# Kernel tuning notes

Measured on AMD Instinct MI355X. Metric: run time of the kernel, lower is better.

The kernel has to match this reference:

```python
import jax, jax.numpy as jnp
import numpy as np
from jax import lax

B, H, W = 16, 512, 512
K, C, D = 64, 512, 256  # num_clusters, feature channels, descriptor_dim


def conv2d(x, w, b, stride, pad):
    y = lax.conv_general_dilated(x, w, (stride, stride), ((pad, pad), (pad, pad)),
                                 dimension_numbers=("NCHW", "OIHW", "NCHW"))
    return y + b[None, :, None, None]


def maxpool2(x):
    return lax.reduce_window(x, -jnp.inf, lax.max, (1, 1, 2, 2), (1, 1, 2, 2), "VALID")


def setup_inputs() -> dict:
    key = jax.random.key(0)
    ks = jax.random.split(key, 16)
    def rn(k, shape, fan_in):
        return jax.random.normal(k, shape, jnp.float32) * (1.0 / np.sqrt(fan_in))
    return {
        "x": jax.random.normal(ks[0], (B, 3, H, W), jnp.float32),
        "w1": rn(ks[1], (64, 3, 3, 3), 27), "b1": jnp.zeros((64,), jnp.float32),
        "w2": rn(ks[2], (128, 64, 3, 3), 576), "b2": jnp.zeros((128,), jnp.float32),
        "w3": rn(ks[3], (256, 128, 3, 3), 1152), "b3": jnp.zeros((256,), jnp.float32),
        "w4": rn(ks[4], (512, 256, 3, 3), 2304), "b4": jnp.zeros((512,), jnp.float32),
        "wv": rn(ks[5], (K, C), C), "bv": jnp.zeros((K,), jnp.float32),
        "centroids": jax.random.normal(ks[6], (K, C), jnp.float32),
        "fw1": rn(ks[7], (D, K * C), K * C), "fb1": jnp.zeros((D,), jnp.float32),
        "fw2": rn(ks[8], (D, D), D), "fb2": jnp.zeros((D,), jnp.float32),
    }


def reference(x, w1, b1, w2, b2, w3, b3, w4, b4, wv, bv, centroids, fw1, fb1, fw2, fb2):
    # conv backbone (SimpleGlobalDescriptor.backbone)
    h = jax.nn.relu(conv2d(x, w1, b1, 2, 1)); h = maxpool2(h)
    h = jax.nn.relu(conv2d(h, w2, b2, 2, 1)); h = maxpool2(h)
    h = jax.nn.relu(conv2d(h, w3, b3, 2, 1)); h = maxpool2(h)
    h = jax.nn.relu(conv2d(h, w4, b4, 2, 1))
    feats = jnp.mean(h, axis=(2, 3))  # AdaptiveAvgPool2d((1,1)) -> (B, C)
    # NetVLAD soft assignment: 1x1 conv + softmax over cluster dim
    logits = jnp.einsum("bc,kc->bk", feats, wv) + bv  # (B, K)
    a = jax.nn.softmax(logits, axis=1)  # spatial N == 1 after avgpool
    # fused VLAD: a[:,k] * (feats - centroids[k]) summed over N(=1)
    # == a (outer) feats - a[:,:,None] * centroids
    vlad = a[:, :, None] * (feats[:, None, :] - centroids[None, :, :])  # (B, K, C)
    v = vlad.reshape(B, K * C)
    # final descriptor MLP + L2 norm
    d = jax.nn.relu(v @ fw1.T + fb1) @ fw2.T + fb2
    d = d / jnp.linalg.norm(d, axis=1, keepdims=True)
    return d
```

## Files before the change

kernel.cpp:

```cpp
#include <hip/hip_runtime.h>
#include <hip/hip_bf16.h>

typedef unsigned short ushort_t;
typedef short bf16x8 __attribute__((ext_vector_type(8)));
typedef float f32x4 __attribute__((ext_vector_type(4)));

__device__ __forceinline__ ushort_t f2b(float f) {
    __hip_bfloat16 h = __float2bfloat16(f);
    return *reinterpret_cast<ushort_t*>(&h);
}
__device__ __forceinline__ float b2f(short v) {
    union { unsigned int u; float f; } cv;
    cv.u = ((unsigned int)(ushort_t)v) << 16;
    return cv.f;
}

__global__ __launch_bounds__(256) void k_packall(const float* __restrict__ w1,
                                                 const float* __restrict__ w2,
                                                 const float* __restrict__ w3,
                                                 const float* __restrict__ w4,
                                                 ushort_t* __restrict__ o1,
                                                 ushort_t* __restrict__ o2,
                                                 ushort_t* __restrict__ o3,
                                                 ushort_t* __restrict__ o4m) {
    const int bx = blockIdx.x;
    if (bx < 512) {
        const int co = bx;
        __shared__ float sw[2304];
        for (int i = threadIdx.x; i < 2304; i += 256) sw[i] = w4[(size_t)co * 2304 + i];
        __syncthreads();
        const int g = co >> 4, l15 = co & 15;
        for (int it = threadIdx.x; it < 288; it += 256) {
            const int kc = it >> 2, kg = it & 3;
            const int k0 = kc * 32 + kg * 8;
            const int tap = k0 >> 8, ci0 = k0 & 255;
            const int lane = kg * 16 + l15;
            ushort_t tmp[8];
#pragma unroll
            for (int j = 0; j < 8; ++j)
                tmp[j] = f2b(sw[(ci0 + j) * 9 + tap]);
            *(float4*)(o4m + ((size_t)(kc * 32 + g) * 64 + lane) * 8) = *(const float4*)tmp;
        }
    } else if (bx < 656) {
        const int slot = (bx - 512) * 256 + threadIdx.x;
        const int lane = slot & 63, g = (slot >> 6) & 15, kc = slot >> 10;
        const int k0 = kc * 32 + ((lane >> 4) << 3);
        const int tap = k0 >> 7, cib = k0 & 127;
        const int ky = tap >= 6 ? 2 : (tap >= 3 ? 1 : 0), kx = tap - ky * 3;
        const int co = g * 16 + (lane & 15);
#pragma unroll
        for (int j = 0; j < 8; ++j)
            o3[slot * 8 + j] = f2b(w3[((co * 128 + cib + j) * 3 + ky) * 3 + kx]);
    } else if (bx < 692) {
        const int slot = (bx - 656) * 256 + threadIdx.x;
        const int lane = slot & 63, g = (slot >> 6) & 7, kc = slot >> 9;
        const int k0 = kc * 32 + ((lane >> 4) << 3);
        const int tap = k0 >> 6, sb = k0 & 63;
        const int ky = tap >= 6 ? 2 : (tap >= 3 ? 1 : 0), kx = tap - ky * 3;
        const int co = g * 16 + (lane & 15);
#pragma unroll
        for (int j = 0; j < 8; ++j) {
            const int s = sb + j;
            const int ci = 16 * (s & 3) + (s >> 2);
            o2[slot * 8 + j] = f2b(w2[((co * 64 + ci) * 3 + ky) * 3 + kx]);
        }
    } else {
        const int slot = threadIdx.x;
        const int lane = slot & 63, nf = slot >> 6;
        const int co = nf * 16 + (lane & 15);
        const int kg = lane >> 4;
#pragma unroll
        for (int j = 0; j < 8; ++j) {
            const int k = kg * 8 + j;
            float v = 0.f;
            if (k < 27) {
                const int t = k / 3, c = k - 3 * t;
                v = w1[(co * 3 + c) * 9 + t];
            }
            o1[slot * 8 + j] = f2b(v);
        }
    }
}

__global__ __launch_bounds__(256) void k_conv1f(const float* __restrict__ x,
                                                const ushort_t* __restrict__ wpk1,
                                                const float* __restrict__ b1,
                                                ushort_t* __restrict__ y1) {
    const int rp = blockIdx.x, xh = blockIdx.y, b = blockIdx.z;
    const int tid = threadIdx.x;
    const int wid = tid >> 6, lane = tid & 63;
    const int l15 = lane & 15, kg = lane >> 4;

    __shared__ __align__(16) ushort_t sX[3 * 9 * 260];
    const float* xb = x + (size_t)b * 3 * 512 * 512;
    const int iy0 = 8 * rp - 1;
    const int ix0 = 256 * xh - 1;
#pragma unroll
    for (int c = 0; c < 3; ++c)
#pragma unroll
    for (int r = 0; r < 9; ++r) {
        const int iy = iy0 + r;
        const int ix = ix0 + tid;
        float v = 0.f;
        if (iy >= 0 && ix >= 0) v = xb[((size_t)c * 512 + iy) * 512 + ix];
        sX[(c * 9 + r) * 260 + tid] = f2b(v);
    }
    if (tid < 27) {
        const int c = tid / 9, r = tid - 9 * c;
        const int iy = iy0 + r, ix = ix0 + 256;
        float v = (iy >= 0) ? xb[((size_t)c * 512 + iy) * 512 + ix] : 0.f;
        sX[(c * 9 + r) * 260 + 256] = f2b(v);
    }
    __syncthreads();

    const int kbase = kg * 8;
#define OFFJ(J) __extension__ ({ int k_ = kbase + (J); if (k_ > 26) k_ = 26; \
        const int tap_ = k_ / 3; const int c_ = k_ - 3 * tap_; \
        const int ky_ = tap_ / 3; const int kx_ = tap_ - 3 * ky_; \
        c_ * 2340 + ky_ * 260 + kx_; })
    const int o0 = OFFJ(0), o1 = OFFJ(1), o2 = OFFJ(2), o3 = OFFJ(3);
    const int o4 = OFFJ(4), o5 = OFFJ(5), o6 = OFFJ(6), o7 = OFFJ(7);
#undef OFFJ
    const int gq = l15 >> 2;
    const int dy = (l15 >> 1) & 1, dx = l15 & 1;

    bf16x8 bF[4];
    float bias[4];
#pragma unroll
    for (int nf = 0; nf < 4; ++nf) {
        bF[nf] = *reinterpret_cast<const bf16x8*>(wpk1 + (size_t)(nf * 64 + lane) * 8);
        bias[nf] = b1[nf * 16 + l15];
    }
    const f32x4 z4 = {0.f, 0.f, 0.f, 0.f};

#pragma unroll 4
    for (int it = 0; it < 8; ++it) {
        const int fl = wid * 8 + it;
        const int g2 = fl * 4 + gq;
        const int pyl = g2 >> 6, pxl = g2 & 63;
        const int cr = 2 * pyl + dy;
        const int oxl = 2 * pxl + dx;
        const int base = cr * 520 + 2 * oxl;
        bf16x8 aF;
        aF[0] = (short)sX[base + o0];
        aF[1] = (short)sX[base + o1];
        aF[2] = (short)sX[base + o2];
        aF[3] = (short)sX[base + o3];
        aF[4] = (short)sX[base + o4];
        aF[5] = (short)sX[base + o5];
        aF[6] = (short)sX[base + o6];
        aF[7] = (short)sX[base + o7];
        f32x4 acc[4];
#pragma unroll
        for (int nf = 0; nf < 4; ++nf)
            acc[nf] = __builtin_amdgcn_mfma_f32_16x16x32_bf16(aF, bF[nf], z4, 0, 0, 0);
        const int g_out = fl * 4 + kg;
        const int pyo = g_out >> 6, pxo = xh * 64 + (g_out & 63);
        union { ushort_t u[4]; uint2 v; } pk;
#pragma unroll
        for (int nf = 0; nf < 4; ++nf) {
            float v = fmaxf(fmaxf(acc[nf][0], acc[nf][1]), fmaxf(acc[nf][2], acc[nf][3]));
            pk.u[nf] = f2b(fmaxf(v + bias[nf], 0.f));
        }
        *(uint2*)(y1 + ((size_t)(b * 128 + 2 * rp + pyo) * 128 + pxo) * 64 + 4 * l15) = pk.v;
    }
}

__global__ __launch_bounds__(256) void k_conv2s(const ushort_t* __restrict__ y1,
                                                const ushort_t* __restrict__ wpk2,
                                                const float* __restrict__ b2,
                                                ushort_t* __restrict__ y2) {
    const int b = blockIdx.z;
    const int xh = blockIdx.y;
    const int rp = blockIdx.x;
    const int tid = threadIdx.x;
    const int wid = tid >> 6, lane = tid & 63;
    const int l15 = lane & 15, kg = lane >> 4;

    __shared__ __align__(16) ushort_t sY[330 * 72];
    bf16x8* sYv = (bf16x8*)sY;

    const ushort_t* xb = y1 + (size_t)b * 128 * 128 * 64;
    const int iyb = 4 * rp - 1, ixb = 64 * xh - 1;
    for (int j = tid; j < 2640; j += 256) {
        const int q = j & 7;
        const int pc = j >> 3;
        const int cc = pc % 66, r = pc / 66;
        const int iy = iyb + r, ix = ixb + cc;
        bf16x8 v = {0, 0, 0, 0, 0, 0, 0, 0};
        if (iy >= 0 && ix >= 0 && ix < 128)
            v = *reinterpret_cast<const bf16x8*>(xb + ((size_t)iy * 128 + ix) * 64 + q * 8);
        sYv[pc * 9 + (q ^ ((pc >> 1) & 7))] = v;
    }
    __syncthreads();

    const f32x4 z4 = {0.f, 0.f, 0.f, 0.f};
    f32x4 acc[2][2][2];
#pragma unroll
    for (int i = 0; i < 2; ++i)
#pragma unroll
        for (int j = 0; j < 2; ++j) { acc[i][j][0] = z4; acc[i][j][1] = z4; }

#pragma unroll 1
    for (int tap = 0; tap < 9; ++tap) {
        const int ky = tap >= 6 ? 2 : (tap >= 3 ? 1 : 0), kx = tap - ky * 3;
#pragma unroll
        for (int h = 0; h < 2; ++h) {
            const int kc = tap * 2 + h;
            const int c8 = h * 4 + kg;
            bf16x8 aF[2][2];
#pragma unroll
            for (int oyi = 0; oyi < 2; ++oyi)
#pragma unroll
            for (int m2 = 0; m2 < 2; ++m2) {
                const int r = 2 * oyi + ky;
                const int cc = 2 * l15 + m2 * 32 + kx;
                const int pc = r * 66 + cc;
                aF[oyi][m2] = sYv[pc * 9 + (c8 ^ ((pc >> 1) & 7))];
            }
            bf16x8 bF[2];
#pragma unroll
            for (int nf = 0; nf < 2; ++nf)
                bF[nf] = *reinterpret_cast<const bf16x8*>(wpk2 + ((size_t)(kc * 8 + wid * 2 + nf) * 64 + lane) * 8);
#pragma unroll
            for (int oyi = 0; oyi < 2; ++oyi)
#pragma unroll
            for (int m2 = 0; m2 < 2; ++m2)
#pragma unroll
            for (int nf = 0; nf < 2; ++nf)
                acc[oyi][m2][nf] = __builtin_amdgcn_mfma_f32_16x16x32_bf16(aF[oyi][m2], bF[nf], acc[oyi][m2][nf], 0, 0, 0);
        }
    }
    const int kgx = lane >> 4;
#pragma unroll
    for (int nf = 0; nf < 2; ++nf) {
        const int co = wid * 32 + nf * 16 + l15;
        const float bias = b2[co];
#pragma unroll
        for (int m2 = 0; m2 < 2; ++m2)
#pragma unroll
            for (int p = 0; p < 2; ++p) {
                float v = fmaxf(fmaxf(acc[0][m2][nf][2 * p], acc[0][m2][nf][2 * p + 1]),
                                fmaxf(acc[1][m2][nf][2 * p], acc[1][m2][nf][2 * p + 1]));
                const int px = (xh * 2 + m2) * 8 + kgx * 2 + p;
                y2[((size_t)(b * 32 + rp) * 32 + px) * 128 + co] = f2b(fmaxf(v + bias, 0.f));
            }
    }
}

__global__ __launch_bounds__(256) void k_conv3m(const ushort_t* __restrict__ y2,
                                                const ushort_t* __restrict__ wpk3,
                                                const float* __restrict__ b3,
                                                ushort_t* __restrict__ y3) {
    const int gy = blockIdx.x, gn = blockIdx.y, b = blockIdx.z;
    const int oy0 = gy * 4;
    const int tid = threadIdx.x;
    const int wid = tid >> 6, lane = tid & 63;
    const int l15 = lane & 15, kl8 = (lane >> 4) << 3;
    const int g16 = gn * 4 + wid;
    const int co = g16 * 16 + l15;

    const ushort_t* xb = y2 + (size_t)b * 32 * 32 * 128;
    const f32x4 z4 = {0.f, 0.f, 0.f, 0.f};
    f32x4 acc[4] = {z4, z4, z4, z4};

#pragma unroll 1
    for (int tap = 0; tap < 9; ++tap) {
        const int ky = tap >= 6 ? 2 : (tap >= 3 ? 1 : 0), kx = tap - ky * 3;
        const int iyA = 2 * oy0 - 1 + ky;
        const int c = 2 * l15 - 1 + kx;
        const bool cok = (c >= 0);
#pragma unroll
        for (int h = 0; h < 4; ++h) {
            const int ci0 = h * 32;
            const int kc = tap * 4 + h;
            bf16x8 aF[4];
#pragma unroll
            for (int mf = 0; mf < 4; ++mf) {
                const int iy = iyA + 2 * mf;
                bf16x8 r = {0, 0, 0, 0, 0, 0, 0, 0};
                if (cok && iy >= 0) r = *reinterpret_cast<const bf16x8*>(xb + ((size_t)iy * 32 + c) * 128 + ci0 + kl8);
                aF[mf] = r;
            }
            const bf16x8 bF = *reinterpret_cast<const bf16x8*>(wpk3 + ((size_t)(kc * 16 + g16) * 64 + lane) * 8);
#pragma unroll
            for (int mf = 0; mf < 4; ++mf)
                acc[mf] = __builtin_amdgcn_mfma_f32_16x16x32_bf16(aF[mf], bF, acc[mf], 0, 0, 0);
        }
    }
    const int kg = lane >> 4;
    const float bias = b3[co];
#pragma unroll
    for (int mp = 0; mp < 2; ++mp) {
        const int py = gy * 2 + mp;
#pragma unroll
        for (int p = 0; p < 2; ++p) {
            float v = fmaxf(fmaxf(acc[2 * mp][2 * p], acc[2 * mp][2 * p + 1]),
                            fmaxf(acc[2 * mp + 1][2 * p], acc[2 * mp + 1][2 * p + 1]));
            const int px = kg * 2 + p;
            y3[((size_t)(b * 8 + py) * 8 + px) * 256 + co] = f2b(fmaxf(v + bias, 0.f));
        }
    }
}

__global__ __launch_bounds__(256) void k_conv4g(const ushort_t* __restrict__ y3,
                                                const ushort_t* __restrict__ wpk4m,
                                                const float* __restrict__ b4,
                                                float* __restrict__ feats) {
    const int g16 = blockIdx.x, b = blockIdx.y;
    const int tid = threadIdx.x, wid = tid >> 6, lane = tid & 63;
    const int l15 = lane & 15, kg = lane >> 4, kl8 = kg << 3;
    const int oy = l15 >> 2, ox = l15 & 3;
    const f32x4 z4 = {0.f, 0.f, 0.f, 0.f};
    f32x4 acc = z4;
    const ushort_t* yb = y3 + (size_t)b * 16384;
    const int kc0 = wid * 18;

#pragma unroll 3
    for (int i = 0; i < 18; ++i) {
        const int kc = kc0 + i;
        const int k0 = kc * 32 + kl8;
        const int tap = k0 >> 8, ci0 = k0 & 255;
        const int ky = tap / 3, kx = tap - 3 * (tap / 3);
        const int iy = 2 * oy - 1 + ky, ix = 2 * ox - 1 + kx;
        bf16x8 aF = {0, 0, 0, 0, 0, 0, 0, 0};
        if (iy >= 0 && ix >= 0)
            aF = *reinterpret_cast<const bf16x8*>(yb + ((iy * 8 + ix) << 8) + ci0);
        const bf16x8 bF = *reinterpret_cast<const bf16x8*>(wpk4m + ((size_t)(kc * 32 + g16) * 64 + lane) * 8);
        acc = __builtin_amdgcn_mfma_f32_16x16x32_bf16(aF, bF, acc, 0, 0, 0);
    }

    __shared__ f32x4 red[4][64];
    red[wid][lane] = acc;
    __syncthreads();
    if (wid == 0) {
        f32x4 t = red[0][lane];
        t = t + red[1][lane];
        t = t + red[2][lane];
        t = t + red[3][lane];
        const int co = g16 * 16 + l15;
        const float bias = b4[co];
        float s = fmaxf(t[0] + bias, 0.f) + fmaxf(t[1] + bias, 0.f)
                + fmaxf(t[2] + bias, 0.f) + fmaxf(t[3] + bias, 0.f);
        s += __shfl_xor(s, 16, 64);
        s += __shfl_xor(s, 32, 64);
        if (kg == 0) feats[b * 512 + co] = s * 0.0625f;
    }
}

__global__ __launch_bounds__(256) void k_head(const float* __restrict__ feats,
                                              const float* __restrict__ wv,
                                              const float* __restrict__ bv,
                                              const float* __restrict__ centroids,
                                              float* __restrict__ v) {
    const int b = blockIdx.x, sl8 = blockIdx.y;
    __shared__ float sf[512];
    __shared__ float sl[64];
    __shared__ float sa[64];
    for (int i = threadIdx.x; i < 512; i += 256) sf[i] = feats[b * 512 + i];
    __syncthreads();
    if (threadIdx.x < 64) {
        const int k = threadIdx.x;
        float s = bv[k];
        for (int c = 0; c < 512; ++c) s += sf[c] * wv[(size_t)k * 512 + c];
        sl[k] = s;
    }
    __syncthreads();
    if (threadIdx.x < 64) {
        const int k = threadIdx.x;
        float m = -1e30f;
        for (int i = 0; i < 64; ++i) m = fmaxf(m, sl[i]);
        float sum = 0.f;
        for (int i = 0; i < 64; ++i) sum += __expf(sl[i] - m);
        sa[k] = __expf(sl[k] - m) / sum;
    }
    __syncthreads();
    const int i4end = (sl8 + 1) * 4096;
    for (int i4 = sl8 * 4096 + threadIdx.x * 4; i4 < i4end; i4 += 1024) {
        const int k = i4 >> 9;
        const float a_ = sa[k];
        const float4 c4 = *(const float4*)(centroids + i4);
        const float4 f4 = *(const float4*)(&sf[i4 & 511]);
        float4 o;
        o.x = a_ * (f4.x - c4.x);
        o.y = a_ * (f4.y - c4.y);
        o.z = a_ * (f4.z - c4.z);
        o.w = a_ * (f4.w - c4.w);
        *(float4*)(v + (size_t)b * 32768 + i4) = o;
    }
}

__global__ __launch_bounds__(256) void k_fc1m(const float* __restrict__ v,
                                              const float* __restrict__ fw1,
                                              float* __restrict__ part) {
    const int g16 = blockIdx.x, by = blockIdx.y;
    const int tid = threadIdx.x, wid = tid >> 6, lane = tid & 63;
    const int l15 = lane & 15, kg = lane >> 4;
    const f32x4 z4 = {0.f, 0.f, 0.f, 0.f};
    f32x4 acc = z4;
    const float* vrow = v + (size_t)l15 * 32768;
    const float* wrow = fw1 + (size_t)(g16 * 16 + l15) * 32768;
    const int kc0 = by * 16 + wid * 4;

#pragma unroll
    for (int i = 0; i < 4; ++i) {
        const int j0 = (kc0 + i) * 32 + kg * 8;
        const float4 va = *(const float4*)(vrow + j0);
        const float4 vb = *(const float4*)(vrow + j0 + 4);
        const float4 wa = *(const float4*)(wrow + j0);
        const float4 wb = *(const float4*)(wrow + j0 + 4);
        bf16x8 aF, bF;
        aF[0] = (short)f2b(va.x); aF[1] = (short)f2b(va.y);
        aF[2] = (short)f2b(va.z); aF[3] = (short)f2b(va.w);
        aF[4] = (short)f2b(vb.x); aF[5] = (short)f2b(vb.y);
        aF[6] = (short)f2b(vb.z); aF[7] = (short)f2b(vb.w);
        bF[0] = (short)f2b(wa.x); bF[1] = (short)f2b(wa.y);
        bF[2] = (short)f2b(wa.z); bF[3] = (short)f2b(wa.w);
        bF[4] = (short)f2b(wb.x); bF[5] = (short)f2b(wb.y);
        bF[6] = (short)f2b(wb.z); bF[7] = (short)f2b(wb.w);
        acc = __builtin_amdgcn_mfma_f32_16x16x32_bf16(aF, bF, acc, 0, 0, 0);
    }

    __shared__ f32x4 red[4][64];
    red[wid][lane] = acc;
    __syncthreads();
    if (wid == 0) {
        f32x4 t = red[0][lane];
        t = t + red[1][lane];
        t = t + red[2][lane];
        t = t + red[3][lane];
#pragma unroll
        for (int r = 0; r < 4; ++r)
            part[((size_t)by * 16 + (kg * 4 + r)) * 256 + g16 * 16 + l15] = t[r];
    }
}

__global__ __launch_bounds__(256) void k_fc2(const float* __restrict__ part,
                                             const float* __restrict__ fb1,
                                             const float* __restrict__ fw2,
                                             const float* __restrict__ fb2,
                                             float* __restrict__ out) {
    const int b = blockIdx.x;
    const int dd = threadIdx.x;
    __shared__ float sd[256];
    __shared__ float sq[256];
    float t = fb1[dd];
#pragma unroll 8
    for (int ks = 0; ks < 64; ++ks) t += part[((size_t)ks * 16 + b) * 256 + dd];
    sd[dd] = fmaxf(t, 0.f);
    __syncthreads();
    float s = fb2[dd];
    for (int j = 0; j < 256; ++j) s += sd[j] * fw2[(size_t)dd * 256 + j];
    sq[dd] = s * s;
    __syncthreads();
    for (int off = 128; off >= 1; off >>= 1) {
        if (dd < off) sq[dd] += sq[dd + off];
        __syncthreads();
    }
    const float inv = rsqrtf(sq[0]);
    out[b * 256 + dd] = s * inv;
}

extern "C" void kernel_launch(void* const* d_in, const int* in_sizes, int n_in,
                              void* d_out, int out_size, void* d_ws, size_t ws_size,
                              hipStream_t stream) {
    const float* x    = (const float*)d_in[0];
    const float* w1   = (const float*)d_in[1];
    const float* b1   = (const float*)d_in[2];
    const float* w2   = (const float*)d_in[3];
    const float* b2   = (const float*)d_in[4];
    const float* w3   = (const float*)d_in[5];
    const float* b3   = (const float*)d_in[6];
    const float* w4   = (const float*)d_in[7];
    const float* b4   = (const float*)d_in[8];
    const float* wv   = (const float*)d_in[9];
    const float* bv   = (const float*)d_in[10];
    const float* cen  = (const float*)d_in[11];
    const float* fw1  = (const float*)d_in[12];
    const float* fb1  = (const float*)d_in[13];
    const float* fw2  = (const float*)d_in[14];
    const float* fb2  = (const float*)d_in[15];
    float* out = (float*)d_out;

    char* p = (char*)d_ws;
    ushort_t* y1    = (ushort_t*)p; p += 33554432;
    ushort_t* wpk2  = (ushort_t*)p; p += 147456;
    ushort_t* wpk3  = (ushort_t*)p; p += 589824;
    ushort_t* wpk4m = (ushort_t*)p; p += 2359296;
    ushort_t* wpk1  = (ushort_t*)p; p += 4096;
    ushort_t* y2    = (ushort_t*)p; p += 4194304;
    ushort_t* y3    = (ushort_t*)p; p += 524288;
    float*    feats = (float*)p;    p += 32768;
    float*    vbuf  = (float*)p;    p += 2097152;
    float*    part  = (float*)p;    p += 1048576;

    k_packall<<<693, 256, 0, stream>>>(w1, w2, w3, w4, wpk1, wpk2, wpk3, wpk4m);
    k_conv1f<<<dim3(64, 2, 16), 256, 0, stream>>>(x, wpk1, b1, y1);
    k_conv2s<<<dim3(32, 2, 16), 256, 0, stream>>>(y1, wpk2, b2, y2);
    k_conv3m<<<dim3(4, 4, 16), 256, 0, stream>>>(y2, wpk3, b3, y3);
    k_conv4g<<<dim3(32, 16), 256, 0, stream>>>(y3, wpk4m, b4, feats);
    k_head<<<dim3(16, 8), 256, 0, stream>>>(feats, wv, bv, cen, vbuf);
    k_fc1m<<<dim3(16, 64), 256, 0, stream>>>(vbuf, fw1, part);
    k_fc2<<<16, 256, 0, stream>>>(part, fb1, fw2, fb2, out);
}
```

Baseline: 115.4 us.

## Interleave conv1 input channels in LDS and store VLAD vector as bf16

Conv1's shared-memory tile now interleaves the three input channels per pixel, and the packed weight K ordering is reordered to (ky, kx, c). Each MFMA A fragment is then read with four 32-bit loads from contiguous LDS instead of eight scattered 16-bit gathers, with a special path for the three leftover taps. Separately, the VLAD head writes bf16 instead of fp32, which halves that buffer's traffic and drops the conversion in fc1. The risk is extra divergence in the kg==3 branch and possible unaligned 32-bit LDS reads at odd offsets.

```diff
diff --git a/kernel.cpp b/kernel.cpp
--- a/kernel.cpp
+++ b/kernel.cpp
@@ -73,9 +73,13 @@
         for (int j = 0; j < 8; ++j) {
             const int k = kg * 8 + j;
             float v = 0.f;
-            if (k < 27) {
-                const int t = k / 3, c = k - 3 * t;
-                v = w1[(co * 3 + c) * 9 + t];
+            if (k < 24) {
+                const int ky = k >> 3, q = k & 7;
+                const int kx = q / 3, c = q - 3 * kx;
+                v = w1[(co * 3 + c) * 9 + ky * 3 + kx];
+            } else if (k < 27) {
+                const int ky = k - 24;
+                v = w1[(co * 3 + 2) * 9 + ky * 3 + 2];
             }
             o1[slot * 8 + j] = f2b(v);
         }
@@ -91,7 +95,7 @@
     const int wid = tid >> 6, lane = tid & 63;
     const int l15 = lane & 15, kg = lane >> 4;
 
-    __shared__ __align__(16) ushort_t sX[3 * 9 * 260];
+    __shared__ __align__(16) ushort_t sX[9 * 776];
     const float* xb = x + (size_t)b * 3 * 512 * 512;
     const int iy0 = 8 * rp - 1;
     const int ix0 = 256 * xh - 1;
@@ -103,24 +107,16 @@
         const int ix = ix0 + tid;
         float v = 0.f;
         if (iy >= 0 && ix >= 0) v = xb[((size_t)c * 512 + iy) * 512 + ix];
-        sX[(c * 9 + r) * 260 + tid] = f2b(v);
+        sX[r * 776 + tid * 3 + c] = f2b(v);
     }
     if (tid < 27) {
         const int c = tid / 9, r = tid - 9 * c;
         const int iy = iy0 + r, ix = ix0 + 256;
         float v = (iy >= 0) ? xb[((size_t)c * 512 + iy) * 512 + ix] : 0.f;
-        sX[(c * 9 + r) * 260 + 256] = f2b(v);
-    }
-    __syncthreads();
-
-    const int kbase = kg * 8;
-#define OFFJ(J) __extension__ ({ int k_ = kbase + (J); if (k_ > 26) k_ = 26; \
-        const int tap_ = k_ / 3; const int c_ = k_ - 3 * tap_; \
-        const int ky_ = tap_ / 3; const int kx_ = tap_ - 3 * ky_; \
-        c_ * 2340 + ky_ * 260 + kx_; })
-    const int o0 = OFFJ(0), o1 = OFFJ(1), o2 = OFFJ(2), o3 = OFFJ(3);
-    const int o4 = OFFJ(4), o5 = OFFJ(5), o6 = OFFJ(6), o7 = OFFJ(7);
-#undef OFFJ
+        sX[r * 776 + 256 * 3 + c] = f2b(v);
+    }
+    __syncthreads();
+
     const int gq = l15 >> 2;
     const int dy = (l15 >> 1) & 1, dx = l15 & 1;
 
@@ -140,16 +136,20 @@
         const int pyl = g2 >> 6, pxl = g2 & 63;
         const int cr = 2 * pyl + dy;
         const int oxl = 2 * pxl + dx;
-        const int base = cr * 520 + 2 * oxl;
         bf16x8 aF;
-        aF[0] = (short)sX[base + o0];
-        aF[1] = (short)sX[base + o1];
-        aF[2] = (short)sX[base + o2];
-        aF[3] = (short)sX[base + o3];
-        aF[4] = (short)sX[base + o4];
-        aF[5] = (short)sX[base + o5];
-        aF[6] = (short)sX[base + o6];
-        aF[7] = (short)sX[base + o7];
+        if (kg < 3) {
+            const int ba = (2 * cr + kg) * 776 + 6 * oxl;
+            const unsigned int* pu = (const unsigned int*)(sX + ba);
+            union { unsigned int u[4]; bf16x8 v; } cvt;
+            cvt.u[0] = pu[0]; cvt.u[1] = pu[1]; cvt.u[2] = pu[2]; cvt.u[3] = pu[3];
+            aF = cvt.v;
+        } else {
+            const int b0 = 2 * cr * 776 + 6 * oxl + 8;
+            aF = (bf16x8){0, 0, 0, 0, 0, 0, 0, 0};
+            aF[0] = (short)sX[b0];
+            aF[1] = (short)sX[b0 + 776];
+            aF[2] = (short)sX[b0 + 1552];
+        }
         f32x4 acc[4];
 #pragma unroll
         for (int nf = 0; nf < 4; ++nf)
@@ -352,7 +352,7 @@
                                               const float* __restrict__ wv,
                                               const float* __restrict__ bv,
                                               const float* __restrict__ centroids,
-                                              float* __restrict__ v) {
+                                              ushort_t* __restrict__ v) {
     const int b = blockIdx.x, sl8 = blockIdx.y;
     __shared__ float sf[512];
     __shared__ float sl[64];
@@ -381,16 +381,16 @@
         const float a_ = sa[k];
         const float4 c4 = *(const float4*)(centroids + i4);
         const float4 f4 = *(const float4*)(&sf[i4 & 511]);
-        float4 o;
-        o.x = a_ * (f4.x - c4.x);
-        o.y = a_ * (f4.y - c4.y);
-        o.z = a_ * (f4.z - c4.z);
-        o.w = a_ * (f4.w - c4.w);
-        *(float4*)(v + (size_t)b * 32768 + i4) = o;
-    }
-}
-
-__global__ __launch_bounds__(256) void k_fc1m(const float* __restrict__ v,
+        union { ushort_t u[4]; uint2 w; } pk;
+        pk.u[0] = f2b(a_ * (f4.x - c4.x));
+        pk.u[1] = f2b(a_ * (f4.y - c4.y));
+        pk.u[2] = f2b(a_ * (f4.z - c4.z));
+        pk.u[3] = f2b(a_ * (f4.w - c4.w));
+        *(uint2*)(v + (size_t)b * 32768 + i4) = pk.w;
+    }
+}
+
+__global__ __launch_bounds__(256) void k_fc1m(const ushort_t* __restrict__ v,
                                               const float* __restrict__ fw1,
                                               float* __restrict__ part) {
     const int g16 = blockIdx.x, by = blockIdx.y;
@@ -398,22 +398,17 @@
     const int l15 = lane & 15, kg = lane >> 4;
     const f32x4 z4 = {0.f, 0.f, 0.f, 0.f};
     f32x4 acc = z4;
-    const float* vrow = v + (size_t)l15 * 32768;
+    const ushort_t* vrow = v + (size_t)l15 * 32768;
     const float* wrow = fw1 + (size_t)(g16 * 16 + l15) * 32768;
     const int kc0 = by * 16 + wid * 4;
 
 #pragma unroll
     for (int i = 0; i < 4; ++i) {
         const int j0 = (kc0 + i) * 32 + kg * 8;
-        const float4 va = *(const float4*)(vrow + j0);
-        const float4 vb = *(const float4*)(vrow + j0 + 4);
+        const bf16x8 aF = *reinterpret_cast<const bf16x8*>(vrow + j0);
         const float4 wa = *(const float4*)(wrow + j0);
         const float4 wb = *(const float4*)(wrow + j0 + 4);
-        bf16x8 aF, bF;
-        aF[0] = (short)f2b(va.x); aF[1] = (short)f2b(va.y);
-        aF[2] = (short)f2b(va.z); aF[3] = (short)f2b(va.w);
-        aF[4] = (short)f2b(vb.x); aF[5] = (short)f2b(vb.y);
-        aF[6] = (short)f2b(vb.z); aF[7] = (short)f2b(vb.w);
+        bf16x8 bF;
         bF[0] = (short)f2b(wa.x); bF[1] = (short)f2b(wa.y);
         bF[2] = (short)f2b(wa.z); bF[3] = (short)f2b(wa.w);
         bF[4] = (short)f2b(wb.x); bF[5] = (short)f2b(wb.y);
@@ -491,7 +486,7 @@
     ushort_t* y2    = (ushort_t*)p; p += 4194304;
     ushort_t* y3    = (ushort_t*)p; p += 524288;
     float*    feats = (float*)p;    p += 32768;
-    float*    vbuf  = (float*)p;    p += 2097152;
+    ushort_t* vbuf  = (ushort_t*)p; p += 1048576;
     float*    part  = (float*)p;    p += 1048576;
 
     k_packall<<<693, 256, 0, stream>>>(w1, w2, w3, w4, wpk1, wpk2, wpk3, wpk4m);
```

Result: faster. 111.8 us, median of 2 (-3.1%).
